# Optimization experiments

Hardware: AMD Instinct MI355X
Metric: run time of the kernel (lower is better)

## Reference

```python
import jax, jax.numpy as jnp
import numpy as np

EPS = 1e-5

def conv2d(x, w, pad):
    # x: [B,C,H,W], w: [O,I,kh,kw]
    return jax.lax.conv_general_dilated(x, w, window_strides=(1, 1),
                                        padding=[(pad, pad), (pad, pad)],
                                        dimension_numbers=('NCHW', 'OIHW', 'NCHW'))

def bn(x, g, b, m, v):
    # inference-mode BatchNorm2d
    scale = g / jnp.sqrt(v + EPS)
    return x * scale[None, :, None, None] + (b - m * scale)[None, :, None, None]

def setup_inputs() -> dict:
    key = jax.random.key(0)
    ks = jax.random.split(key, 12)
    B, C, H, W = 4, 256, 300, 300
    HC, NC, NREG = 64, 3, 8
    inp = {
        'bev_features': jax.random.normal(ks[0], (B, C, H, W), jnp.float32),
        'w_shared': jax.random.normal(ks[1], (HC, C, 3, 3), jnp.float32) * 0.02,
        'g_shared': jax.random.uniform(ks[2], (HC,), jnp.float32, 0.5, 1.5),
        'b_shared': jnp.zeros((HC,), jnp.float32),
        'm_shared': jnp.zeros((HC,), jnp.float32),
        'v_shared': jnp.ones((HC,), jnp.float32),
        'w_hm1': jax.random.normal(ks[3], (HC, HC, 3, 3), jnp.float32) * 0.05,
        'g_hm1': jax.random.uniform(ks[4], (HC,), jnp.float32, 0.5, 1.5),
        'b_hm1': jnp.zeros((HC,), jnp.float32),
        'm_hm1': jnp.zeros((HC,), jnp.float32),
        'v_hm1': jnp.ones((HC,), jnp.float32),
        'w_hm2': jax.random.normal(ks[5], (NC, HC, 1, 1), jnp.float32) * 0.05,
        'b_hm2': jnp.full((NC,), -2.19, jnp.float32),  # focal-loss prior init
        'w_reg1': jax.random.normal(ks[6], (HC, HC, 3, 3), jnp.float32) * 0.05,
        'g_reg1': jax.random.uniform(ks[7], (HC,), jnp.float32, 0.5, 1.5),
        'b_reg1': jnp.zeros((HC,), jnp.float32),
        'm_reg1': jnp.zeros((HC,), jnp.float32),
        'v_reg1': jnp.ones((HC,), jnp.float32),
        'w_reg2': jax.random.normal(ks[8], (NREG, HC, 1, 1), jnp.float32) * 0.05,
        'b_reg2': jnp.zeros((NREG,), jnp.float32),
    }
    return inp

def reference(bev_features, w_shared, g_shared, b_shared, m_shared, v_shared,
              w_hm1, g_hm1, b_hm1, m_hm1, v_hm1, w_hm2, b_hm2,
              w_reg1, g_reg1, b_reg1, m_reg1, v_reg1, w_reg2, b_reg2):
    # shared trunk: conv3x3 -> BN -> ReLU
    shared = jax.nn.relu(bn(conv2d(bev_features, w_shared, 1), g_shared, b_shared, m_shared, v_shared))
    # heatmap head: conv3x3 -> BN -> ReLU -> conv1x1(+bias)
    hm = jax.nn.relu(bn(conv2d(shared, w_hm1, 1), g_hm1, b_hm1, m_hm1, v_hm1))
    heatmap = conv2d(hm, w_hm2, 0) + b_hm2[None, :, None, None]
    rg = jax.nn.relu(bn(conv2d(shared, w_reg1, 1), g_reg1, b_reg1, m_reg1, v_reg1))
    box_reg = conv2d(rg, w_reg2, 0) + b_reg2[None, :, None, None]
    return heatmap, box_reg
```

## Files before the change

### kernel.cpp

```cpp
#include <hip/hip_runtime.h>


typedef __attribute__((ext_vector_type(8))) short bf16x8;
typedef __attribute__((ext_vector_type(4))) float f32x4;

#define WIMG 300
#define HW 90000
#define NWG 1500

__device__ __forceinline__ unsigned short f2bf(float f) {
    unsigned u = __float_as_uint(f);
    u += 0x7fff + ((u >> 16) & 1);
    return (unsigned short)(u >> 16);
}

__device__ __forceinline__ void gload16(const unsigned short* g, unsigned short* l) {
    __builtin_amdgcn_global_load_lds(
        (const __attribute__((address_space(1))) void*)g,
        (__attribute__((address_space(3))) void*)l, 16, 0, 0);
}

__device__ __forceinline__ void swz_block(int& bx, int& by, int& bz) {
    const int orig = blockIdx.x + 5 * (blockIdx.y + 75 * blockIdx.z);
    const int q = NWG / 8, r = NWG % 8;
    const int xcd = orig & 7, i = orig >> 3;
    const int wg = (xcd < r) ? xcd * (q + 1) + i
                             : r * (q + 1) + (xcd - r) * q + i;
    bx = wg % 5;
    const int rest = wg / 5;
    by = rest % 75;
    bz = rest / 75;
}

__global__ __launch_bounds__(256) void nchw2nhwc_bf16_k(
    const float* __restrict__ in_all,
    unsigned short* __restrict__ out_all)
{
    __shared__ unsigned short lds[32][132];
    const int p0 = blockIdx.x * 128;
    const int c0 = blockIdx.y * 32;
    const int b = blockIdx.z;
    const float* in = in_all + (size_t)b * 256 * HW;
    unsigned short* out = out_all + (size_t)b * HW * 256;
    const int t = threadIdx.x;

#pragma unroll
    for (int i = 0; i < 4; ++i) {
        int task = i * 256 + t;
        int c = task >> 5;
        int p4 = (task & 31) * 4;
        const float* src = in + (size_t)(c0 + c) * HW + p0 + p4;
        float4 v;
        if (p0 + p4 + 3 < HW) {
            v = *(const float4*)src;
        } else {
            v.x = (p0 + p4 + 0 < HW) ? src[0] : 0.f;
            v.y = (p0 + p4 + 1 < HW) ? src[1] : 0.f;
            v.z = (p0 + p4 + 2 < HW) ? src[2] : 0.f;
            v.w = (p0 + p4 + 3 < HW) ? src[3] : 0.f;
        }
        uint2 pk;
        pk.x = (unsigned)f2bf(v.x) | ((unsigned)f2bf(v.y) << 16);
        pk.y = (unsigned)f2bf(v.z) | ((unsigned)f2bf(v.w) << 16);
        *(uint2*)&lds[c][p4] = pk;
    }
    __syncthreads();

    const int ct = t & 7;
    const int pt = t >> 3;
    uint2 r[4];
#pragma unroll
    for (int j = 0; j < 4; ++j)
        r[j] = *(const uint2*)&lds[ct * 4 + j][pt * 4];
#pragma unroll
    for (int i = 0; i < 4; ++i) {
        unsigned e0 = (((i < 2) ? r[0].x : r[0].y) >> ((i & 1) * 16)) & 0xffffu;
        unsigned e1 = (((i < 2) ? r[1].x : r[1].y) >> ((i & 1) * 16)) & 0xffffu;
        unsigned e2 = (((i < 2) ? r[2].x : r[2].y) >> ((i & 1) * 16)) & 0xffffu;
        unsigned e3 = (((i < 2) ? r[3].x : r[3].y) >> ((i & 1) * 16)) & 0xffffu;
        uint2 o;
        o.x = e0 | (e1 << 16);
        o.y = e2 | (e3 << 16);
        int px = p0 + pt * 4 + i;
        if (px < HW)
            *(uint2*)&out[(size_t)px * 256 + c0 + ct * 4] = o;
    }
}

__global__ __launch_bounds__(256) void pack_w_k(
    const float* __restrict__ w, unsigned short* __restrict__ apack, int CIN)
{
    const int KSUB = CIN / 32;
    const int tot = 9 * KSUB * 4 * 64 * 8;
    int idx = blockIdx.x * 256 + threadIdx.x;
    if (idx >= tot) return;
    int j = idx & 7;
    int lane = (idx >> 3) & 63;
    int rest = idx >> 9;
    int mt = rest & 3;
    int rest2 = rest >> 2;
    int ks = rest2 % KSUB;
    int tap = rest2 / KSUB;
    int oc = mt * 16 + (lane & 15);
    int ic = ks * 32 + (lane >> 4) * 8 + j;
    apack[idx] = f2bf(w[((size_t)oc * CIN + ic) * 9 + tap]);
}

#define TASKS (396 * 4)

template <int CIN>
__device__ __forceinline__ void make_sp(const unsigned short* inb,
                                        const unsigned short* zp,
                                        int x0, int y0, int wave, int lane,
                                        const unsigned short* (&sp)[7]) {
#pragma unroll
    for (int i = 0; i < 7; ++i) {
        int task = i * 256 + wave * 64 + lane;
        int s = task & 3;
        int px = task >> 2;
        int r = px / 66;
        int c = px - r * 66;
        int ys = y0 - 1 + r;
        int xs = x0 - 1 + c;
        bool ok = (task < TASKS) && ((unsigned)ys < (unsigned)WIMG)
                                 && ((unsigned)xs < (unsigned)WIMG);
        sp[i] = ok ? (inb + ((size_t)ys * WIMG + xs) * CIN + s * 8) : zp;
    }
}

__device__ __forceinline__ void stage_ks(const unsigned short* const (&sp)[7],
                                         uint4* dst, int wave, int ks) {
#pragma unroll
    for (int i = 0; i < 7; ++i) {
        int base = i * 256 + wave * 64;
        if (base < TASKS)
            gload16(sp[i] + ks * 32, (unsigned short*)&dst[base]);
    }
}

__global__ __launch_bounds__(256, 3) void conv3_trunk_k(
    const unsigned short* __restrict__ in_all,
    const uint4* __restrict__ apack,
    const float* __restrict__ gg, const float* __restrict__ bb,
    const float* __restrict__ mm, const float* __restrict__ vv,
    unsigned short* __restrict__ out_nhwc_all,
    const unsigned short* __restrict__ zp)
{
    constexpr int CIN = 256, KSUB = 8;
    __shared__ uint4 lds4[2][1600];

    const int wave = threadIdx.x >> 6;
    const int lane = threadIdx.x & 63;
    const int n16 = lane & 15;
    const int quad = lane >> 4;
    int bx, by, b;
    swz_block(bx, by, b);
    const int x0 = bx * 64;
    const int y0 = by * 4;
    const int y = y0 + wave;
    const unsigned short* inb = in_all + (size_t)b * HW * CIN;

    const unsigned short* sp[7];
    make_sp<CIN>(inb, zp, x0, y0, wave, lane, sp);

    f32x4 acc[4][4];
#pragma unroll
    for (int mt = 0; mt < 4; ++mt)
#pragma unroll
        for (int nt = 0; nt < 4; ++nt)
            acc[mt][nt] = (f32x4){0.f, 0.f, 0.f, 0.f};

    union U16 { uint4 u; bf16x8 h; };

    stage_ks(sp, lds4[0], wave, 0);
    asm volatile("s_waitcnt vmcnt(0)" ::: "memory");
    __syncthreads();

    int cur = 0;
#pragma unroll 1
    for (int ks = 0; ks < KSUB; ++ks) {
        if (ks + 1 < KSUB)
            stage_ks(sp, lds4[cur ^ 1], wave, ks + 1);
        const unsigned short* lp = (const unsigned short*)lds4[cur];
#pragma unroll
        for (int tap = 0; tap < 9; ++tap) {
            const int dy = tap / 3 - 1, dx = tap % 3 - 1;
            const int rbase = (wave + dy + 1) * 66 + dx + 1;
            U16 bf[4], a[4];
#pragma unroll
            for (int nt = 0; nt < 4; ++nt)
                bf[nt].u = *(const uint4*)(lp + (size_t)(rbase + nt * 16 + n16) * 32 + quad * 8);
#pragma unroll
            for (int mt = 0; mt < 4; ++mt)
                a[mt].u = apack[(size_t)(((tap * KSUB + ks) * 4 + mt) * 64) + lane];
#pragma unroll
            for (int mt = 0; mt < 4; ++mt)
#pragma unroll
                for (int nt = 0; nt < 4; ++nt)
                    acc[mt][nt] = __builtin_amdgcn_mfma_f32_16x16x32_bf16(
                        a[mt].h, bf[nt].h, acc[mt][nt], 0, 0, 0);
        }
        asm volatile("s_waitcnt vmcnt(0)" ::: "memory");
        __syncthreads();
        cur ^= 1;
    }

    float scl[4][4], sft[4][4];
#pragma unroll
    for (int mt = 0; mt < 4; ++mt)
#pragma unroll
        for (int j = 0; j < 4; ++j) {
            int c = mt * 16 + quad * 4 + j;
            float s = gg[c] / sqrtf(vv[c] + 1e-5f);
            scl[mt][j] = s;
            sft[mt][j] = bb[c] - mm[c] * s;
        }

    unsigned short* outb = out_nhwc_all + (size_t)b * HW * 64;
#pragma unroll
    for (int nt = 0; nt < 4; ++nt) {
        int xg = x0 + nt * 16 + n16;
        if (xg < WIMG) {
            unsigned short* op = outb + ((size_t)y * WIMG + xg) * 64 + quad * 4;
#pragma unroll
            for (int mt = 0; mt < 4; ++mt) {
                union { unsigned short s[4]; uint2 u; } pk;
#pragma unroll
                for (int j = 0; j < 4; ++j) {
                    float t = acc[mt][nt][j] * scl[mt][j] + sft[mt][j];
                    pk.s[j] = f2bf(t > 0.f ? t : 0.f);
                }
                *(uint2*)(op + mt * 16) = pk.u;
            }
        }
    }
}

__global__ __launch_bounds__(256, 2) void conv3_dualhead_k(
    const unsigned short* __restrict__ in_all,
    const uint4* __restrict__ apack_h,
    const uint4* __restrict__ apack_r,
    const float* __restrict__ g_h, const float* __restrict__ b_h,
    const float* __restrict__ m_h, const float* __restrict__ v_h,
    const float* __restrict__ g_r, const float* __restrict__ b_r,
    const float* __restrict__ m_r, const float* __restrict__ v_r,
    const float* __restrict__ w2_h, const float* __restrict__ b2_h,
    const float* __restrict__ w2_r, const float* __restrict__ b2_r,
    float* __restrict__ out_h_all,
    float* __restrict__ out_r_all,
    const unsigned short* __restrict__ zp)
{
    constexpr int CIN = 64, KSUB = 2;
    __shared__ uint4 lds4[2][1600];

    const int wave = threadIdx.x >> 6;
    const int lane = threadIdx.x & 63;
    const int n16 = lane & 15;
    const int quad = lane >> 4;
    int bx, by, b;
    swz_block(bx, by, b);
    const int x0 = bx * 64;
    const int y0 = by * 4;
    const int y = y0 + wave;
    const unsigned short* inb = in_all + (size_t)b * HW * CIN;

    const unsigned short* sp[7];
    make_sp<CIN>(inb, zp, x0, y0, wave, lane, sp);

    f32x4 acch[4][4], accr[4][4];
#pragma unroll
    for (int mt = 0; mt < 4; ++mt)
#pragma unroll
        for (int nt = 0; nt < 4; ++nt) {
            acch[mt][nt] = (f32x4){0.f, 0.f, 0.f, 0.f};
            accr[mt][nt] = (f32x4){0.f, 0.f, 0.f, 0.f};
        }

    union U16 { uint4 u; bf16x8 h; };

    stage_ks(sp, lds4[0], wave, 0);
    asm volatile("s_waitcnt vmcnt(0)" ::: "memory");
    __syncthreads();

    int cur = 0;
#pragma unroll 1
    for (int ks = 0; ks < KSUB; ++ks) {
        if (ks + 1 < KSUB)
            stage_ks(sp, lds4[cur ^ 1], wave, ks + 1);
        const unsigned short* lp = (const unsigned short*)lds4[cur];
#pragma unroll
        for (int tap = 0; tap < 9; ++tap) {
            const int dy = tap / 3 - 1, dx = tap % 3 - 1;
            const int rbase = (wave + dy + 1) * 66 + dx + 1;
            U16 bf[4];
#pragma unroll
            for (int nt = 0; nt < 4; ++nt)
                bf[nt].u = *(const uint4*)(lp + (size_t)(rbase + nt * 16 + n16) * 32 + quad * 8);
#pragma unroll
            for (int mt = 0; mt < 4; ++mt) {
                U16 ah, ar;
                size_t ai = (size_t)(((tap * KSUB + ks) * 4 + mt) * 64) + lane;
                ah.u = apack_h[ai];
                ar.u = apack_r[ai];
#pragma unroll
                for (int nt = 0; nt < 4; ++nt) {
                    acch[mt][nt] = __builtin_amdgcn_mfma_f32_16x16x32_bf16(
                        ah.h, bf[nt].h, acch[mt][nt], 0, 0, 0);
                    accr[mt][nt] = __builtin_amdgcn_mfma_f32_16x16x32_bf16(
                        ar.h, bf[nt].h, accr[mt][nt], 0, 0, 0);
                }
            }
        }
        asm volatile("s_waitcnt vmcnt(0)" ::: "memory");
        __syncthreads();
        cur ^= 1;
    }

    auto epi = [&](f32x4 (&acc)[4][4], const float* gg, const float* bb,
                   const float* mm, const float* vv, const float* w2,
                   const float* b2, int NOUT, float* outb) {
        float scl[4][4], sft[4][4];
#pragma unroll
        for (int mt = 0; mt < 4; ++mt)
#pragma unroll
            for (int j = 0; j < 4; ++j) {
                int c = mt * 16 + quad * 4 + j;
                float s = gg[c] / sqrtf(vv[c] + 1e-5f);
                scl[mt][j] = s;
                sft[mt][j] = bb[c] - mm[c] * s;
            }
#pragma unroll
        for (int mt = 0; mt < 4; ++mt)
#pragma unroll
            for (int nt = 0; nt < 4; ++nt)
#pragma unroll
                for (int j = 0; j < 4; ++j) {
                    float t = acc[mt][nt][j] * scl[mt][j] + sft[mt][j];
                    acc[mt][nt][j] = t > 0.f ? t : 0.f;
                }
        for (int no = 0; no < NOUT; ++no) {
            float wv[4][4];
#pragma unroll
            for (int mt = 0; mt < 4; ++mt)
#pragma unroll
                for (int j = 0; j < 4; ++j)
                    wv[mt][j] = w2[no * 64 + mt * 16 + quad * 4 + j];
#pragma unroll
            for (int nt = 0; nt < 4; ++nt) {
                float s = 0.f;
#pragma unroll
                for (int mt = 0; mt < 4; ++mt)
#pragma unroll
                    for (int j = 0; j < 4; ++j)
                        s += acc[mt][nt][j] * wv[mt][j];
                s += __shfl_xor(s, 16);
                s += __shfl_xor(s, 32);
                int xg = x0 + nt * 16 + n16;
                if (((no & 3) == quad) && xg < WIMG)
                    outb[(size_t)no * HW + (size_t)y * WIMG + xg] = s + b2[no];
            }
        }
    };

    epi(acch, g_h, b_h, m_h, v_h, w2_h, b2_h, 3, out_h_all + (size_t)b * 3 * HW);
    epi(accr, g_r, b_r, m_r, v_r, w2_r, b2_r, 8, out_r_all + (size_t)b * 8 * HW);
}

extern "C" void kernel_launch(void* const* d_in, const int* in_sizes, int n_in,
                              void* d_out, int out_size, void* d_ws, size_t ws_size,
                              hipStream_t stream) {
    const float* bev    = (const float*)d_in[0];
    const float* w_sh   = (const float*)d_in[1];
    const float* g_sh   = (const float*)d_in[2];
    const float* b_sh   = (const float*)d_in[3];
    const float* m_sh   = (const float*)d_in[4];
    const float* v_sh   = (const float*)d_in[5];
    const float* w_hm1  = (const float*)d_in[6];
    const float* g_hm1  = (const float*)d_in[7];
    const float* b_hm1  = (const float*)d_in[8];
    const float* m_hm1  = (const float*)d_in[9];
    const float* v_hm1  = (const float*)d_in[10];
    const float* w_hm2  = (const float*)d_in[11];
    const float* b_hm2  = (const float*)d_in[12];
    const float* w_reg1 = (const float*)d_in[13];
    const float* g_reg1 = (const float*)d_in[14];
    const float* b_reg1 = (const float*)d_in[15];
    const float* m_reg1 = (const float*)d_in[16];
    const float* v_reg1 = (const float*)d_in[17];
    const float* w_reg2 = (const float*)d_in[18];
    const float* b_reg2 = (const float*)d_in[19];

    char* ws = (char*)d_ws;
    unsigned short* inbuf     = (unsigned short*)(ws);
    unsigned short* sharedbuf = (unsigned short*)(ws + 184320000);
    unsigned short* apk1      = (unsigned short*)(ws + 230400000);
    unsigned short* apkh      = (unsigned short*)(ws + 230694912);
    unsigned short* apkr      = (unsigned short*)(ws + 230768640);
    unsigned short* zp        = (unsigned short*)(ws + 230842368);

    float* heatmap = (float*)d_out;
    float* box_reg = heatmap + (size_t)4 * 3 * HW;

    hipMemsetAsync(zp, 0, 4096, stream);

    pack_w_k<<<dim3(576), 256, 0, stream>>>(w_sh, apk1, 256);
    pack_w_k<<<dim3(144), 256, 0, stream>>>(w_hm1, apkh, 64);
    pack_w_k<<<dim3(144), 256, 0, stream>>>(w_reg1, apkr, 64);

    nchw2nhwc_bf16_k<<<dim3(704, 8, 4), 256, 0, stream>>>(bev, inbuf);

    const dim3 cgrid(5, 75, 4);
    conv3_trunk_k<<<cgrid, 256, 0, stream>>>(
        inbuf, (const uint4*)apk1, g_sh, b_sh, m_sh, v_sh, sharedbuf, zp);
    conv3_dualhead_k<<<cgrid, 256, 0, stream>>>(
        sharedbuf, (const uint4*)apkh, (const uint4*)apkr,
        g_hm1, b_hm1, m_hm1, v_hm1,
        g_reg1, b_reg1, m_reg1, v_reg1,
        w_hm2, b_hm2, w_reg2, b_reg2,
        heatmap, box_reg, zp);
}
```

Before: 816.1 us.

## Use 32x32x16 MFMA in trunk conv, single-stage dualhead staging, fuse prep kernels

The trunk conv switches from 16x16x32 to 32x32x16 bf16 MFMA tiles, with the weight packing and LDS read pattern reorganized to match. Larger tiles mean fewer LDS and A-fragment loads per FLOP, at the cost of a different accumulator layout in the epilogue. The dualhead kernel now loads both 32-channel K slices into LDS in one pass instead of double-buffering, which removes a barrier and loop but uses twice the LDS per stage. The three weight-pack launches and the memset are merged into one prep kernel to cut launch overhead.

```diff
diff --git a/kernel.cpp b/kernel.cpp
--- a/kernel.cpp
+++ b/kernel.cpp
@@ -3,6 +3,7 @@
 
 typedef __attribute__((ext_vector_type(8))) short bf16x8;
 typedef __attribute__((ext_vector_type(4))) float f32x4;
+typedef __attribute__((ext_vector_type(16))) float f32x16;
 
 #define WIMG 300
 #define HW 90000
@@ -87,32 +88,69 @@
     }
 }
 
-__global__ __launch_bounds__(256) void pack_w_k(
-    const float* __restrict__ w, unsigned short* __restrict__ apack, int CIN)
+__global__ __launch_bounds__(256) void prep_k(
+    const float* __restrict__ w_sh, const float* __restrict__ w_hm,
+    const float* __restrict__ w_rg,
+    unsigned short* __restrict__ apk1, unsigned short* __restrict__ apkh,
+    unsigned short* __restrict__ apkr, unsigned short* __restrict__ zp)
 {
-    const int KSUB = CIN / 32;
-    const int tot = 9 * KSUB * 4 * 64 * 8;
-    int idx = blockIdx.x * 256 + threadIdx.x;
-    if (idx >= tot) return;
-    int j = idx & 7;
-    int lane = (idx >> 3) & 63;
-    int rest = idx >> 9;
-    int mt = rest & 3;
-    int rest2 = rest >> 2;
-    int ks = rest2 % KSUB;
-    int tap = rest2 / KSUB;
-    int oc = mt * 16 + (lane & 15);
-    int ic = ks * 32 + (lane >> 4) * 8 + j;
-    apack[idx] = f2bf(w[((size_t)oc * CIN + ic) * 9 + tap]);
-}
-
-#define TASKS (396 * 4)
-
-template <int CIN>
-__device__ __forceinline__ void make_sp(const unsigned short* inb,
-                                        const unsigned short* zp,
-                                        int x0, int y0, int wave, int lane,
-                                        const unsigned short* (&sp)[7]) {
+    const int blk = blockIdx.x;
+    const int tid = threadIdx.x;
+    if (blk < 576) {
+        int idx = blk * 256 + tid;
+        int j = idx & 7;
+        int lane = (idx >> 3) & 63;
+        int mt = (idx >> 9) & 1;
+        int ks16 = (idx >> 10) & 1;
+        int rest = idx >> 11;
+        int ks32 = rest & 7;
+        int tap = rest >> 3;
+        int oc = mt * 32 + (lane & 31);
+        int ic = ks32 * 32 + ks16 * 16 + (lane >> 5) * 8 + j;
+        apk1[idx] = f2bf(w_sh[((size_t)oc * 256 + ic) * 9 + tap]);
+    } else if (blk < 864) {
+        const float* w = (blk < 720) ? w_hm : w_rg;
+        unsigned short* ap = (blk < 720) ? apkh : apkr;
+        int idx = ((blk < 720) ? (blk - 576) : (blk - 720)) * 256 + tid;
+        int j = idx & 7;
+        int lane = (idx >> 3) & 63;
+        int mt = (idx >> 9) & 3;
+        int rest2 = idx >> 11;
+        int ks = rest2 & 1;
+        int tap = rest2 >> 1;
+        int oc = mt * 16 + (lane & 15);
+        int ic = ks * 32 + (lane >> 4) * 8 + j;
+        ap[idx] = f2bf(w[((size_t)oc * 64 + ic) * 9 + tap]);
+    } else {
+        ((uint4*)zp)[tid] = (uint4){0u, 0u, 0u, 0u};
+    }
+}
+
+#define TASKS 1584
+
+__global__ __launch_bounds__(256, 3) void conv3_trunk_k(
+    const unsigned short* __restrict__ in_all,
+    const uint4* __restrict__ apack,
+    const float* __restrict__ gg, const float* __restrict__ bb,
+    const float* __restrict__ mm, const float* __restrict__ vv,
+    unsigned short* __restrict__ out_nhwc_all,
+    const unsigned short* __restrict__ zp)
+{
+    constexpr int CIN = 256, KSUB = 8;
+    __shared__ uint4 lds4[2][1600];
+
+    const int wave = threadIdx.x >> 6;
+    const int lane = threadIdx.x & 63;
+    const int l31 = lane & 31;
+    const int half = lane >> 5;
+    int bx, by, b;
+    swz_block(bx, by, b);
+    const int x0 = bx * 64;
+    const int y0 = by * 4;
+    const int y = y0 + wave;
+    const unsigned short* inb = in_all + (size_t)b * HW * CIN;
+
+    const unsigned short* sp[7];
 #pragma unroll
     for (int i = 0; i < 7; ++i) {
         int task = i * 256 + wave * 64 + lane;
@@ -126,53 +164,26 @@
                                  && ((unsigned)xs < (unsigned)WIMG);
         sp[i] = ok ? (inb + ((size_t)ys * WIMG + xs) * CIN + s * 8) : zp;
     }
-}
-
-__device__ __forceinline__ void stage_ks(const unsigned short* const (&sp)[7],
-                                         uint4* dst, int wave, int ks) {
-#pragma unroll
-    for (int i = 0; i < 7; ++i) {
-        int base = i * 256 + wave * 64;
-        if (base < TASKS)
-            gload16(sp[i] + ks * 32, (unsigned short*)&dst[base]);
-    }
-}
-
-__global__ __launch_bounds__(256, 3) void conv3_trunk_k(
-    const unsigned short* __restrict__ in_all,
-    const uint4* __restrict__ apack,
-    const float* __restrict__ gg, const float* __restrict__ bb,
-    const float* __restrict__ mm, const float* __restrict__ vv,
-    unsigned short* __restrict__ out_nhwc_all,
-    const unsigned short* __restrict__ zp)
-{
-    constexpr int CIN = 256, KSUB = 8;
-    __shared__ uint4 lds4[2][1600];
-
-    const int wave = threadIdx.x >> 6;
-    const int lane = threadIdx.x & 63;
-    const int n16 = lane & 15;
-    const int quad = lane >> 4;
-    int bx, by, b;
-    swz_block(bx, by, b);
-    const int x0 = bx * 64;
-    const int y0 = by * 4;
-    const int y = y0 + wave;
-    const unsigned short* inb = in_all + (size_t)b * HW * CIN;
-
-    const unsigned short* sp[7];
-    make_sp<CIN>(inb, zp, x0, y0, wave, lane, sp);
-
-    f32x4 acc[4][4];
-#pragma unroll
-    for (int mt = 0; mt < 4; ++mt)
-#pragma unroll
-        for (int nt = 0; nt < 4; ++nt)
-            acc[mt][nt] = (f32x4){0.f, 0.f, 0.f, 0.f};
+
+    f32x16 acc[2][2];
+#pragma unroll
+    for (int mt = 0; mt < 2; ++mt)
+#pragma unroll
+        for (int nt = 0; nt < 2; ++nt)
+            acc[mt][nt] = (f32x16){0.f};
 
     union U16 { uint4 u; bf16x8 h; };
 
-    stage_ks(sp, lds4[0], wave, 0);
+    auto stage = [&](int buf, int ks) {
+#pragma unroll
+        for (int i = 0; i < 7; ++i) {
+            int base = i * 256 + wave * 64;
+            if (base < TASKS)
+                gload16(sp[i] + ks * 32, (unsigned short*)&lds4[buf][base]);
+        }
+    };
+
+    stage(0, 0);
     asm volatile("s_waitcnt vmcnt(0)" ::: "memory");
     __syncthreads();
 
@@ -180,61 +191,74 @@
 #pragma unroll 1
     for (int ks = 0; ks < KSUB; ++ks) {
         if (ks + 1 < KSUB)
-            stage_ks(sp, lds4[cur ^ 1], wave, ks + 1);
+            stage(cur ^ 1, ks + 1);
         const unsigned short* lp = (const unsigned short*)lds4[cur];
 #pragma unroll
         for (int tap = 0; tap < 9; ++tap) {
             const int dy = tap / 3 - 1, dx = tap % 3 - 1;
             const int rbase = (wave + dy + 1) * 66 + dx + 1;
-            U16 bf[4], a[4];
-#pragma unroll
-            for (int nt = 0; nt < 4; ++nt)
-                bf[nt].u = *(const uint4*)(lp + (size_t)(rbase + nt * 16 + n16) * 32 + quad * 8);
-#pragma unroll
-            for (int mt = 0; mt < 4; ++mt)
-                a[mt].u = apack[(size_t)(((tap * KSUB + ks) * 4 + mt) * 64) + lane];
-#pragma unroll
-            for (int mt = 0; mt < 4; ++mt)
-#pragma unroll
-                for (int nt = 0; nt < 4; ++nt)
-                    acc[mt][nt] = __builtin_amdgcn_mfma_f32_16x16x32_bf16(
-                        a[mt].h, bf[nt].h, acc[mt][nt], 0, 0, 0);
+            U16 bf[2][2], a[2][2];
+#pragma unroll
+            for (int nt = 0; nt < 2; ++nt)
+#pragma unroll
+                for (int k16 = 0; k16 < 2; ++k16)
+                    bf[nt][k16].u = *(const uint4*)(
+                        lp + (size_t)(rbase + nt * 32 + l31) * 32 + k16 * 16 + half * 8);
+#pragma unroll
+            for (int mt = 0; mt < 2; ++mt)
+#pragma unroll
+                for (int k16 = 0; k16 < 2; ++k16)
+                    a[mt][k16].u = apack[(size_t)((((tap * KSUB + ks) * 2 + k16) * 2 + mt) * 64) + lane];
+#pragma unroll
+            for (int k16 = 0; k16 < 2; ++k16)
+#pragma unroll
+                for (int mt = 0; mt < 2; ++mt)
+#pragma unroll
+                    for (int nt = 0; nt < 2; ++nt)
+                        acc[mt][nt] = __builtin_amdgcn_mfma_f32_32x32x16_bf16(
+                            a[mt][k16].h, bf[nt][k16].h, acc[mt][nt], 0, 0, 0);
         }
         asm volatile("s_waitcnt vmcnt(0)" ::: "memory");
         __syncthreads();
         cur ^= 1;
     }
 
-    float scl[4][4], sft[4][4];
-#pragma unroll
-    for (int mt = 0; mt < 4; ++mt)
-#pragma unroll
-        for (int j = 0; j < 4; ++j) {
-            int c = mt * 16 + quad * 4 + j;
-            float s = gg[c] / sqrtf(vv[c] + 1e-5f);
-            scl[mt][j] = s;
-            sft[mt][j] = bb[c] - mm[c] * s;
-        }
+    float scl[2][4][4], sft[2][4][4];
+#pragma unroll
+    for (int mt = 0; mt < 2; ++mt)
+#pragma unroll
+        for (int g = 0; g < 4; ++g)
+#pragma unroll
+            for (int j = 0; j < 4; ++j) {
+                int c = mt * 32 + g * 8 + half * 4 + j;
+                float s = gg[c] / sqrtf(vv[c] + 1e-5f);
+                scl[mt][g][j] = s;
+                sft[mt][g][j] = bb[c] - mm[c] * s;
+            }
 
     unsigned short* outb = out_nhwc_all + (size_t)b * HW * 64;
 #pragma unroll
-    for (int nt = 0; nt < 4; ++nt) {
-        int xg = x0 + nt * 16 + n16;
+    for (int nt = 0; nt < 2; ++nt) {
+        int xg = x0 + nt * 32 + l31;
         if (xg < WIMG) {
-            unsigned short* op = outb + ((size_t)y * WIMG + xg) * 64 + quad * 4;
-#pragma unroll
-            for (int mt = 0; mt < 4; ++mt) {
-                union { unsigned short s[4]; uint2 u; } pk;
-#pragma unroll
-                for (int j = 0; j < 4; ++j) {
-                    float t = acc[mt][nt][j] * scl[mt][j] + sft[mt][j];
-                    pk.s[j] = f2bf(t > 0.f ? t : 0.f);
+            unsigned short* op = outb + ((size_t)y * WIMG + xg) * 64;
+#pragma unroll
+            for (int mt = 0; mt < 2; ++mt)
+#pragma unroll
+                for (int g = 0; g < 4; ++g) {
+                    union { unsigned short s[4]; uint2 u; } pk;
+#pragma unroll
+                    for (int j = 0; j < 4; ++j) {
+                        float t = acc[mt][nt][g * 4 + j] * scl[mt][g][j] + sft[mt][g][j];
+                        pk.s[j] = f2bf(t > 0.f ? t : 0.f);
+                    }
+                    *(uint2*)(op + mt * 32 + g * 8 + half * 4) = pk.u;
                 }
-                *(uint2*)(op + mt * 16) = pk.u;
-            }
-        }
-    }
-}
+        }
+    }
+}
+
+#define HTASKS (TASKS * 2)
 
 __global__ __launch_bounds__(256, 2) void conv3_dualhead_k(
     const unsigned short* __restrict__ in_all,
@@ -250,8 +274,7 @@
     float* __restrict__ out_r_all,
     const unsigned short* __restrict__ zp)
 {
-    constexpr int CIN = 64, KSUB = 2;
-    __shared__ uint4 lds4[2][1600];
+    __shared__ uint4 ldsH[3200];
 
     const int wave = threadIdx.x >> 6;
     const int lane = threadIdx.x & 63;
@@ -262,10 +285,24 @@
     const int x0 = bx * 64;
     const int y0 = by * 4;
     const int y = y0 + wave;
-    const unsigned short* inb = in_all + (size_t)b * HW * CIN;
-
-    const unsigned short* sp[7];
-    make_sp<CIN>(inb, zp, x0, y0, wave, lane, sp);
+    const unsigned short* inb = in_all + (size_t)b * HW * 64;
+
+    const unsigned short* sp[13];
+#pragma unroll
+    for (int i = 0; i < 13; ++i) {
+        int task = i * 256 + wave * 64 + lane;
+        int ks = (task >= TASKS) ? 1 : 0;
+        int rr = task - ks * TASKS;
+        int s = rr & 3;
+        int px = rr >> 2;
+        int r = px / 66;
+        int c = px - r * 66;
+        int ys = y0 - 1 + r;
+        int xs = x0 - 1 + c;
+        bool ok = (task < HTASKS) && ((unsigned)ys < (unsigned)WIMG)
+                                  && ((unsigned)xs < (unsigned)WIMG);
+        sp[i] = ok ? (inb + ((size_t)ys * WIMG + xs) * 64 + ks * 32 + s * 8) : zp;
+    }
 
     f32x4 acch[4][4], accr[4][4];
 #pragma unroll
@@ -278,16 +315,18 @@
 
     union U16 { uint4 u; bf16x8 h; };
 
-    stage_ks(sp, lds4[0], wave, 0);
+#pragma unroll
+    for (int i = 0; i < 13; ++i) {
+        int base = i * 256 + wave * 64;
+        if (base < HTASKS)
+            gload16(sp[i], (unsigned short*)&ldsH[base]);
+    }
     asm volatile("s_waitcnt vmcnt(0)" ::: "memory");
     __syncthreads();
 
-    int cur = 0;
-#pragma unroll 1
-    for (int ks = 0; ks < KSUB; ++ks) {
-        if (ks + 1 < KSUB)
-            stage_ks(sp, lds4[cur ^ 1], wave, ks + 1);
-        const unsigned short* lp = (const unsigned short*)lds4[cur];
+#pragma unroll
+    for (int ks = 0; ks < 2; ++ks) {
+        const unsigned short* lp = (const unsigned short*)ldsH + (size_t)ks * (TASKS * 8);
 #pragma unroll
         for (int tap = 0; tap < 9; ++tap) {
             const int dy = tap / 3 - 1, dx = tap % 3 - 1;
@@ -299,7 +338,7 @@
 #pragma unroll
             for (int mt = 0; mt < 4; ++mt) {
                 U16 ah, ar;
-                size_t ai = (size_t)(((tap * KSUB + ks) * 4 + mt) * 64) + lane;
+                size_t ai = (size_t)(((tap * 2 + ks) * 4 + mt) * 64) + lane;
                 ah.u = apack_h[ai];
                 ar.u = apack_r[ai];
 #pragma unroll
@@ -311,9 +350,6 @@
                 }
             }
         }
-        asm volatile("s_waitcnt vmcnt(0)" ::: "memory");
-        __syncthreads();
-        cur ^= 1;
     }
 
     auto epi = [&](f32x4 (&acc)[4][4], const float* gg, const float* bb,
@@ -401,11 +437,7 @@
     float* heatmap = (float*)d_out;
     float* box_reg = heatmap + (size_t)4 * 3 * HW;
 
-    hipMemsetAsync(zp, 0, 4096, stream);
-
-    pack_w_k<<<dim3(576), 256, 0, stream>>>(w_sh, apk1, 256);
-    pack_w_k<<<dim3(144), 256, 0, stream>>>(w_hm1, apkh, 64);
-    pack_w_k<<<dim3(144), 256, 0, stream>>>(w_reg1, apkr, 64);
+    prep_k<<<dim3(865), 256, 0, stream>>>(w_sh, w_hm1, w_reg1, apk1, apkh, apkr, zp);
 
     nchw2nhwc_bf16_k<<<dim3(704, 8, 4), 256, 0, stream>>>(bev, inbuf);
 
```

New measurement: 846.6 us. 3.7% more time.
